# Kernel optimization log

Measured on AMD Instinct MI355X. Metric: run time of the kernel, lower is better.

## Reference

```python
import jax, jax.numpy as jnp
import numpy as np

D = 8        # q_ndim (= dof_ndim)
HID = 200    # hidden_size
N = 16384    # batch of states
EPS = 0.1    # qdot regularizer coefficient in L()


def _lagrangian(z, Ws, bs):
    # z: (2D,) = [q, qdot]; angular_dims=() so CosSin is an identity pass-through
    v = z[D:]
    h = z
    for W, b in zip(Ws[:-1], bs[:-1]):
        h = jax.nn.softplus(h @ W + b)   # FCsoftplus blocks
    L = (h @ Ws[-1] + bs[-1])[0]          # final Linear -> scalar (Reshape(-1))
    return L + EPS * jnp.dot(v, v)


def setup_inputs():
    key = jax.random.key(0)
    ks = jax.random.split(key, 5)
    z = jax.random.normal(ks[0], (N, 2 * D), dtype=jnp.float32)
    t = jnp.zeros((), dtype=jnp.float32)

    def lin(k, fi, fo, scale):
        return (jax.random.normal(k, (fi, fo), dtype=jnp.float32)
                * jnp.float32(scale / np.sqrt(fi)))

    W0 = lin(ks[1], 2 * D, HID, 1.0)
    W1 = lin(ks[2], HID, HID, 1.0)
    W2 = lin(ks[3], HID, HID, 1.0)
    W3 = lin(ks[4], HID, 1, 0.01)  # small head keeps mass matrix M well conditioned
    b0 = jnp.zeros((HID,), jnp.float32)  # zero_bias init per FCsoftplus/Linear
    b1 = jnp.zeros((HID,), jnp.float32)
    b2 = jnp.zeros((HID,), jnp.float32)
    b3 = jnp.zeros((1,), jnp.float32)
    return dict(t=t, z=z, W0=W0, b0=b0, W1=W1, b1=b1, W2=W2, b2=b2, W3=W3, b3=b3)


def reference(t, z, W0, b0, W1, b1, W2, b2, W3, b3):
    # Euler-Lagrange dynamics (LagrangianDynamics):
    #   M a = dL/dq - (d2L/dq dv) v,  M = d2L/dv2;  dz/dt = [v, a]
    Ws = (W0, W1, W2, W3)
    bs = (b0, b1, b2, b3)
    Lfn = lambda zz: _lagrangian(zz, Ws, bs)

    def dyn_single(zi):
        g = jax.grad(Lfn)(zi)              # (2D,)  = [dL/dq, dL/dv]
        H = jax.jacfwd(jax.grad(Lfn))(zi)  # (2D,2D) Hessian of L wrt z
        v = zi[D:]
        M = H[D:, D:]                      # d(dL/dv)/dv  -> mass matrix
        C = H[D:, :D]                      # d(dL/dv)/dq
        F = g[:D] - C @ v
        a = jnp.linalg.solve(M, F)
        return jnp.concatenate([v, a])     # (2D,)

    return jax.vmap(dyn_single)(z)         # (N, 2D)
```

## Files before the change

### kernel.cpp

```cpp
#include <hip/hip_runtime.h>
#include <math.h>

#define DD 8
#define ZD 16
#define HID 200
#define EPSL 0.1f
#define BS 16
#define NTHREADS 1024
#define NKC 7
#define NMT 13
#define XSTR 216
#define CSTR 212
#define HSTR 20
#define WSTR 208
#define NTAN 8
#define NT4 4

#define KSC 1024.0f
#define SSC 64.0f
#define INV_K (1.0f/1024.0f)
#define INV_KS (1.0f/65536.0f)

typedef _Float16 half8 __attribute__((ext_vector_type(8)));
typedef _Float16 half4v __attribute__((ext_vector_type(4)));
typedef _Float16 half2v __attribute__((ext_vector_type(2)));
typedef __fp16 fp16x2 __attribute__((ext_vector_type(2)));
typedef float float4v __attribute__((ext_vector_type(4)));

#define S4 (NKC*NMT*64*8)
#define OFF_W1T 0
#define OFF_W2T (S4)
#define OFF_W1  (2*S4)
#define OFF_W2  (3*S4)
#define OFF_W0T (4*S4)
#define OFF_W0  (4*S4 + NMT*64*8)
#define WS_HALFS (4*S4 + NMT*64*8 + NKC*64*8)

__global__ void prep(const float* __restrict__ W0, const float* __restrict__ W1,
                     const float* __restrict__ W2, _Float16* __restrict__ ws)
{
    int idx = blockIdx.x * 256 + threadIdx.x;
    if (idx >= WS_HALFS) return;
    float v = 0.f;
    if (idx < 4*S4) {
        int arr = idx / S4, e = idx % S4;
        int kc = e / (NMT*64*8); int r = e % (NMT*64*8);
        int mt = r / (64*8); r %= 64*8;
        int lane = r / 8, j = r % 8;
        int m = mt*16 + (lane & 15);
        int k = kc*32 + (lane >> 4)*8 + j;
        if (m < HID && k < HID) {
            if      (arr == 0) v = W1[k*HID + m];
            else if (arr == 1) v = W2[k*HID + m];
            else if (arr == 2) v = W1[m*HID + k];
            else               v = W2[m*HID + k];
        }
    } else if (idx < OFF_W0) {
        int e = idx - OFF_W0T;
        int mt = e / (64*8); int r = e % (64*8);
        int lane = r / 8, j = r % 8;
        int m = mt*16 + (lane & 15);
        int k = (lane >> 4)*8 + j;
        if (m < HID && k < ZD) v = W0[k*HID + m];
    } else {
        int e = idx - OFF_W0;
        int kc = e / (64*8); int r = e % (64*8);
        int lane = r / 8, j = r % 8;
        int m = (lane & 15);
        int k = kc*32 + (lane >> 4)*8 + j;
        if (k < HID) v = W0[m*HID + k];
    }
    ws[idx] = (_Float16)v;
}

__device__ __forceinline__ half4v pk4(float4v a) {
    half2v lo = __builtin_bit_cast(half2v, __builtin_amdgcn_cvt_pkrtz(a.x, a.y));
    half2v hi = __builtin_bit_cast(half2v, __builtin_amdgcn_cvt_pkrtz(a.z, a.w));
    return __builtin_shufflevector(lo, hi, 0, 1, 2, 3);
}
__device__ __forceinline__ void sig_sp(float x, float& sp, float& sg) {
    float e = __expf(-fabsf(x));
    float r = 1.0f / (1.0f + e);
    sg = (x >= 0.f) ? r : (1.0f - r);
    sp = fmaxf(x, 0.f) + __logf(1.f + e);
}

template<int NTILES>
__device__ __forceinline__ void run_mv(const half8* __restrict__ Asw,
                                       const _Float16* __restrict__ Xsrc,
                                       int mt0, int mtc, int lane,
                                       float4v acc[2][NTILES])
{
    const int lm = lane & 15, q = lane >> 4;
#pragma unroll
    for (int m = 0; m < 2; ++m)
#pragma unroll
        for (int n = 0; n < NTILES; ++n)
            acc[m][n] = (float4v){0.f, 0.f, 0.f, 0.f};
    for (int kc = 0; kc < NKC; ++kc) {
        half8 a[2];
#pragma unroll
        for (int m = 0; m < 2; ++m)
            if (m < mtc) a[m] = Asw[(kc*NMT + mt0 + m)*64 + lane];
        half8 x[NTILES];
#pragma unroll
        for (int n = 0; n < NTILES; ++n)
            x[n] = *(const half8*)(Xsrc + (n*16 + lm)*XSTR + kc*32 + q*8);
#pragma unroll
        for (int m = 0; m < 2; ++m)
            if (m < mtc)
#pragma unroll
                for (int n = 0; n < NTILES; ++n)
                    acc[m][n] = __builtin_amdgcn_mfma_f32_16x16x32_f16(a[m], x[n], acc[m][n], 0, 0, 0);
    }
}

__global__ void __launch_bounds__(NTHREADS, 4)
lnn_main(const float* __restrict__ z,
         const float* __restrict__ W0, const float* __restrict__ b0,
         const float* __restrict__ b1, const float* __restrict__ b2,
         const float* __restrict__ W3,
         const _Float16* __restrict__ ws,
         float* __restrict__ out)
{
    __shared__ alignas(16) _Float16 Xt[128*XSTR];
    __shared__ alignas(16) _Float16 Xb[128*XSTR];
    __shared__ alignas(16) _Float16 Cf[5][16*CSTR];
    __shared__ alignas(16) _Float16 Xz[16*40];
    __shared__ alignas(16) _Float16 bsh[4*WSTR];
    __shared__ alignas(16) _Float16 w0t[NTAN*WSTR];
    __shared__ alignas(16) float gsh[16*HSTR];
    __shared__ alignas(16) float Hr[128*HSTR];

    const int tid  = threadIdx.x;
    const int wave = tid >> 6;
    const int lane = tid & 63;
    const int lm   = lane & 15;
    const int q    = lane >> 4;
    const int s0   = blockIdx.x * BS;

    const int twm  = wave >> 1;
    const int twn  = wave & 1;
    const int mt0t = (twm < 5) ? twm*2 : (twm + 5);
    const int mtct = (twm < 5) ? 2 : 1;

    const half8* W1Tsw = (const half8*)(ws + OFF_W1T);
    const half8* W2Tsw = (const half8*)(ws + OFF_W2T);
    const half8* W1sw  = (const half8*)(ws + OFF_W1);
    const half8* W2sw  = (const half8*)(ws + OFF_W2);
    const half8* W0Tsw = (const half8*)(ws + OFF_W0T);
    const half8* W0sw  = (const half8*)(ws + OFF_W0);

    if (tid < 256) {
        int s = tid >> 4, k = tid & 15;
        Xz[s*40 + k]      = (_Float16)z[(s0 + s)*ZD + k];
        Xz[s*40 + 16 + k] = (_Float16)0.f;
    }
    for (int idx = tid; idx < 128*16; idx += NTHREADS) {
        int r = idx >> 4, c = 200 + (idx & 15);
        Xt[r*XSTR + c] = (_Float16)0.f;
        Xb[r*XSTR + c] = (_Float16)0.f;
    }
    for (int idx = tid; idx < 4*WSTR; idx += NTHREADS) {
        int l = idx / WSTR, u = idx % WSTR;
        float v = 0.f;
        if (u < HID) {
            if      (l == 0) v = b0[u];
            else if (l == 1) v = b1[u];
            else if (l == 2) v = b2[u];
            else             v = KSC * W3[u];
        }
        bsh[idx] = (_Float16)v;
    }
    for (int idx = tid; idx < NTAN*WSTR; idx += NTHREADS) {
        int t = idx / WSTR, u = idx % WSTR;
        w0t[idx] = (_Float16)((u < HID) ? SSC * W0[(DD + t)*HID + u] : 0.f);
    }
    __syncthreads();

    float4v acc1[2][1];
    const int ubf = wave*16 + q*4;

    if (wave < NMT) {
        acc1[0][0] = (float4v){0.f,0.f,0.f,0.f};
        half8 xz = *(const half8*)(Xz + lm*40 + q*8);
        half8 a = W0Tsw[wave*64 + lane];
        acc1[0][0] = __builtin_amdgcn_mfma_f32_16x16x32_f16(a, xz, acc1[0][0], 0, 0, 0);
        half4v bb = *(const half4v*)(&bsh[0*WSTR + ubf]);
        float h[4], p[4];
#pragma unroll
        for (int r = 0; r < 4; ++r) {
            float av = acc1[0][0][r] + (float)bb[r];
            sig_sp(av, h[r], p[r]);
        }
        *(half4v*)(&Xt[lm*XSTR + ubf])     = pk4((float4v){h[0],h[1],h[2],h[3]});
        *(half4v*)(&Cf[0][lm*CSTR + ubf])  = pk4((float4v){p[0],p[1],p[2],p[3]});
    }
    __syncthreads();

    if (wave < NMT) run_mv<1>(W1Tsw, Xt, wave, 1, lane, acc1);
    __syncthreads();
    if (wave < NMT) {
        half4v bb = *(const half4v*)(&bsh[1*WSTR + ubf]);
        float h[4], p[4];
#pragma unroll
        for (int r = 0; r < 4; ++r) {
            float av = acc1[0][0][r] + (float)bb[r];
            sig_sp(av, h[r], p[r]);
        }
        *(half4v*)(&Xt[lm*XSTR + ubf])    = pk4((float4v){h[0],h[1],h[2],h[3]});
        *(half4v*)(&Cf[1][lm*CSTR + ubf]) = pk4((float4v){p[0],p[1],p[2],p[3]});
    }
    __syncthreads();

    if (wave < NMT) run_mv<1>(W2Tsw, Xt, wave, 1, lane, acc1);
    __syncthreads();
    if (wave < NMT) {
        half4v bb = *(const half4v*)(&bsh[2*WSTR + ubf]);
        half4v w3 = *(const half4v*)(&bsh[3*WSTR + ubf]);
        float d2[4], c2[4];
#pragma unroll
        for (int r = 0; r < 4; ++r) {
            float av = acc1[0][0][r] + (float)bb[r];
            float e = __expf(-fabsf(av));
            float rr = 1.f / (1.f + e);
            float sg = (av >= 0.f) ? rr : (1.f - rr);
            float wk = (float)w3[r];
            d2[r] = wk * sg;
            c2[r] = wk * sg * (1.f - sg);
        }
        *(half4v*)(&Xt[lm*XSTR + ubf])    = pk4((float4v){d2[0],d2[1],d2[2],d2[3]});
        *(half4v*)(&Cf[2][lm*CSTR + ubf]) = pk4((float4v){c2[0],c2[1],c2[2],c2[3]});
    }
    __syncthreads();

    if (wave < NMT) run_mv<1>(W2sw, Xt, wave, 1, lane, acc1);
    __syncthreads();
    if (wave < NMT) {
        half4v p1 = *(const half4v*)(&Cf[1][lm*CSTR + ubf]);
        half4v u1 = pk4(acc1[0][0]);
        half4v one = {(_Float16)1.f,(_Float16)1.f,(_Float16)1.f,(_Float16)1.f};
        *(half4v*)(&Xt[lm*XSTR + ubf])    = u1 * p1;
        *(half4v*)(&Cf[3][lm*CSTR + ubf]) = u1 * (one - p1);
    }
    __syncthreads();

    if (wave < NMT) run_mv<1>(W1sw, Xt, wave, 1, lane, acc1);
    __syncthreads();
    if (wave < NMT) {
        half4v p0 = *(const half4v*)(&Cf[0][lm*CSTR + ubf]);
        half4v u0 = pk4(acc1[0][0]);
        half4v one = {(_Float16)1.f,(_Float16)1.f,(_Float16)1.f,(_Float16)1.f};
        half4v d0 = u0 * p0;
        *(half4v*)(&Xt[lm*XSTR + ubf])    = d0;
        *(half4v*)(&Cf[4][lm*CSTR + ubf]) = d0 * (one - p0);
    }
    __syncthreads();

    if (wave == 0) {
        float4v g = (float4v){0.f,0.f,0.f,0.f};
        for (int kc = 0; kc < NKC; ++kc) {
            half8 a = W0sw[kc*64 + lane];
            half8 x = *(const half8*)(Xt + lm*XSTR + kc*32 + q*8);
            g = __builtin_amdgcn_mfma_f32_16x16x32_f16(a, x, g, 0, 0, 0);
        }
        float4v gv; gv.x = g.x*INV_K; gv.y = g.y*INV_K; gv.z = g.z*INV_K; gv.w = g.w*INV_K;
        *(float4v*)(&gsh[lm*HSTR + q*4]) = gv;
    } else {
        for (int idx = tid - 64; idx < 128*50; idx += NTHREADS - 64) {
            int row = idx / 50, u = (idx % 50)*4;
            int s = row & 15, t = row >> 4;
            half4v p0 = *(const half4v*)(&Cf[0][s*CSTR + u]);
            half4v w0 = *(const half4v*)(&w0t[t*WSTR + u]);
            *(half4v*)(&Xb[row*XSTR + u]) = p0 * w0;
        }
    }
    __syncthreads();

    float4v acc4[2][NT4];

    run_mv<NT4>(W1Tsw, Xb + twn*64*XSTR, mt0t, mtct, lane, acc4);
    __syncthreads();
#pragma unroll
    for (int m = 0; m < 2; ++m)
        if (m < mtct) {
            const int ub = (mt0t + m)*16 + q*4;
            half4v p1 = *(const half4v*)(&Cf[1][lm*CSTR + ub]);
#pragma unroll
            for (int n = 0; n < NT4; ++n) {
                int row = (twn*NT4 + n)*16 + lm;
                *(half4v*)(&Xt[row*XSTR + ub]) = pk4(acc4[m][n]) * p1;
            }
        }
    __syncthreads();

    run_mv<NT4>(W2Tsw, Xt + twn*64*XSTR, mt0t, mtct, lane, acc4);
    __syncthreads();
#pragma unroll
    for (int m = 0; m < 2; ++m)
        if (m < mtct) {
            const int ub = (mt0t + m)*16 + q*4;
            half4v c2 = *(const half4v*)(&Cf[2][lm*CSTR + ub]);
#pragma unroll
            for (int n = 0; n < NT4; ++n) {
                int row = (twn*NT4 + n)*16 + lm;
                *(half4v*)(&Xb[row*XSTR + ub]) = pk4(acc4[m][n]) * c2;
            }
        }
    __syncthreads();

    run_mv<NT4>(W2sw, Xb + twn*64*XSTR, mt0t, mtct, lane, acc4);
    __syncthreads();
#pragma unroll
    for (int m = 0; m < 2; ++m)
        if (m < mtct) {
            const int ub = (mt0t + m)*16 + q*4;
            half4v p1 = *(const half4v*)(&Cf[1][lm*CSTR + ub]);
            half4v c3 = *(const half4v*)(&Cf[3][lm*CSTR + ub]);
#pragma unroll
            for (int n = 0; n < NT4; ++n) {
                int row = (twn*NT4 + n)*16 + lm;
                half4v th1 = *(const half4v*)(&Xt[row*XSTR + ub]);
                *(half4v*)(&Xb[row*XSTR + ub]) = pk4(acc4[m][n]) * p1 + c3 * th1;
            }
        }
    __syncthreads();

    run_mv<NT4>(W1sw, Xb + twn*64*XSTR, mt0t, mtct, lane, acc4);
    __syncthreads();
#pragma unroll
    for (int m = 0; m < 2; ++m)
        if (m < mtct) {
            const int ub = (mt0t + m)*16 + q*4;
            half4v p0 = *(const half4v*)(&Cf[0][lm*CSTR + ub]);
            half4v c4 = *(const half4v*)(&Cf[4][lm*CSTR + ub]);
#pragma unroll
            for (int n = 0; n < NT4; ++n) {
                int row = (twn*NT4 + n)*16 + lm;
                half4v w0 = *(const half4v*)(&w0t[(twn*NT4 + n)*WSTR + ub]);
                *(half4v*)(&Xt[row*XSTR + ub]) = pk4(acc4[m][n]) * p0 + c4 * w0;
            }
        }
    __syncthreads();

    if (wave < 8) {
        float4v hacc = (float4v){0.f,0.f,0.f,0.f};
        for (int kc = 0; kc < NKC; ++kc) {
            half8 a = W0sw[kc*64 + lane];
            half8 x = *(const half8*)(Xt + (wave*16 + lm)*XSTR + kc*32 + q*8);
            hacc = __builtin_amdgcn_mfma_f32_16x16x32_f16(a, x, hacc, 0, 0, 0);
        }
        int row = wave*16 + lm;
        float4v hv;
        hv.x = hacc.x*INV_KS; hv.y = hacc.y*INV_KS;
        hv.z = hacc.z*INV_KS; hv.w = hacc.w*INV_KS;
        *(float4v*)(&Hr[row*HSTR + q*4]) = hv;
    }
    __syncthreads();

    if (tid < BS) {
        const int s = tid;
        float M[DD][DD], F[DD], v[DD], a[DD];
#pragma unroll
        for (int c = 0; c < DD; ++c) v[c] = z[(s0 + s)*ZD + DD + c];
#pragma unroll
        for (int r = 0; r < DD; ++r) {
            float f = gsh[s*HSTR + r];
#pragma unroll
            for (int c = 0; c < DD; ++c) {
                M[r][c] = Hr[(r*16 + s)*HSTR + DD + c] + ((r == c) ? 2.f*EPSL : 0.f);
                f -= Hr[(r*16 + s)*HSTR + c] * v[c];
            }
            F[r] = f;
        }
#pragma unroll
        for (int col = 0; col < DD; ++col) {
            const float inv = 1.f / M[col][col];
#pragma unroll
            for (int r = col + 1; r < DD; ++r) {
                const float fac = M[r][col] * inv;
#pragma unroll
                for (int c = col + 1; c < DD; ++c) M[r][c] -= fac * M[col][c];
                F[r] -= fac * F[col];
            }
        }
#pragma unroll
        for (int r = DD - 1; r >= 0; --r) {
            float ssum = F[r];
#pragma unroll
            for (int c = r + 1; c < DD; ++c) ssum -= M[r][c] * a[c];
            a[r] = ssum / M[r][r];
        }
        float* op = out + (size_t)(s0 + s)*ZD;
#pragma unroll
        for (int c = 0; c < DD; ++c) { op[c] = v[c]; op[DD + c] = a[c]; }
    }
}

extern "C" void kernel_launch(void* const* d_in, const int* in_sizes, int n_in,
                              void* d_out, int out_size, void* d_ws, size_t ws_size,
                              hipStream_t stream)
{
    const float* z  = (const float*)d_in[1];
    const float* W0 = (const float*)d_in[2];
    const float* b0 = (const float*)d_in[3];
    const float* W1 = (const float*)d_in[4];
    const float* b1 = (const float*)d_in[5];
    const float* W2 = (const float*)d_in[6];
    const float* b2 = (const float*)d_in[7];
    const float* W3 = (const float*)d_in[8];
    float* out = (float*)d_out;
    _Float16* ws = (_Float16*)d_ws;

    const int n = in_sizes[1] / (2*DD);

    prep<<<dim3((WS_HALFS + 255)/256), dim3(256), 0, stream>>>(W0, W1, W2, ws);
    lnn_main<<<dim3(n / BS), dim3(NTHREADS), 0, stream>>>(
        z, W0, b0, b1, b2, W3, ws, out);
}
```

Baseline: 159.9 us.

## Software-pipeline weight and activation loads in MFMA matvec and drop redundant barriers

The MFMA matvec helper is fully unrolled and now prefetches weight fragments several K-chunks ahead and activation fragments one chunk ahead. It is specialised on the M-tile count through a template parameter, so the runtime tile checks disappear. The W0 gradient and Hessian loops preload all weight fragments up front. Three barriers that separated tangent matvecs from their epilogues are removed, because each epilogue writes a buffer no other wave is reading at that point. The extra live registers may cause spills or lower occupancy under the existing launch bounds.

```diff
diff --git a/kernel.cpp b/kernel.cpp
--- a/kernel.cpp
+++ b/kernel.cpp
@@ -24,7 +24,6 @@
 typedef _Float16 half8 __attribute__((ext_vector_type(8)));
 typedef _Float16 half4v __attribute__((ext_vector_type(4)));
 typedef _Float16 half2v __attribute__((ext_vector_type(2)));
-typedef __fp16 fp16x2 __attribute__((ext_vector_type(2)));
 typedef float float4v __attribute__((ext_vector_type(4)));
 
 #define S4 (NKC*NMT*64*8)
@@ -85,33 +84,62 @@
     sp = fmaxf(x, 0.f) + __logf(1.f + e);
 }
 
-template<int NTILES>
+template<int NTILES, int MTC>
 __device__ __forceinline__ void run_mv(const half8* __restrict__ Asw,
                                        const _Float16* __restrict__ Xsrc,
-                                       int mt0, int mtc, int lane,
+                                       int mt0, int lane,
                                        float4v acc[2][NTILES])
 {
     const int lm = lane & 15, q = lane >> 4;
-#pragma unroll
-    for (int m = 0; m < 2; ++m)
+    constexpr int PF = (NTILES > 1) ? 3 : NKC;
+#pragma unroll
+    for (int m = 0; m < MTC; ++m)
 #pragma unroll
         for (int n = 0; n < NTILES; ++n)
             acc[m][n] = (float4v){0.f, 0.f, 0.f, 0.f};
+
+    half8 a[MTC][PF];
+#pragma unroll
+    for (int p = 0; p < PF; ++p)
+#pragma unroll
+        for (int m = 0; m < MTC; ++m)
+            a[m][p] = Asw[(p*NMT + mt0 + m)*64 + lane];
+
+    half8 x[NTILES];
+#pragma unroll
+    for (int n = 0; n < NTILES; ++n)
+        x[n] = *(const half8*)(Xsrc + (n*16 + lm)*XSTR + q*8);
+
+#pragma unroll
     for (int kc = 0; kc < NKC; ++kc) {
-        half8 a[2];
-#pragma unroll
-        for (int m = 0; m < 2; ++m)
-            if (m < mtc) a[m] = Asw[(kc*NMT + mt0 + m)*64 + lane];
-        half8 x[NTILES];
-#pragma unroll
-        for (int n = 0; n < NTILES; ++n)
-            x[n] = *(const half8*)(Xsrc + (n*16 + lm)*XSTR + kc*32 + q*8);
-#pragma unroll
-        for (int m = 0; m < 2; ++m)
-            if (m < mtc)
-#pragma unroll
-                for (int n = 0; n < NTILES; ++n)
-                    acc[m][n] = __builtin_amdgcn_mfma_f32_16x16x32_f16(a[m], x[n], acc[m][n], 0, 0, 0);
+        half8 xn[NTILES];
+        if (kc + 1 < NKC)
+#pragma unroll
+            for (int n = 0; n < NTILES; ++n)
+                xn[n] = *(const half8*)(Xsrc + (n*16 + lm)*XSTR + (kc+1)*32 + q*8);
+        half8 an[MTC];
+        if (kc + PF < NKC)
+#pragma unroll
+            for (int m = 0; m < MTC; ++m)
+                an[m] = Asw[((kc+PF)*NMT + mt0 + m)*64 + lane];
+
+#pragma unroll
+        for (int m = 0; m < MTC; ++m)
+#pragma unroll
+            for (int n = 0; n < NTILES; ++n)
+                acc[m][n] = __builtin_amdgcn_mfma_f32_16x16x32_f16(a[m][0], x[n], acc[m][n], 0, 0, 0);
+
+        if (kc + 1 < NKC) {
+#pragma unroll
+            for (int m = 0; m < MTC; ++m)
+#pragma unroll
+                for (int p = 0; p + 1 < PF; ++p) a[m][p] = a[m][p+1];
+            if (kc + PF < NKC)
+#pragma unroll
+                for (int m = 0; m < MTC; ++m) a[m][PF-1] = an[m];
+#pragma unroll
+            for (int n = 0; n < NTILES; ++n) x[n] = xn[n];
+        }
     }
 }
 
@@ -161,6 +189,10 @@
         Xt[r*XSTR + c] = (_Float16)0.f;
         Xb[r*XSTR + c] = (_Float16)0.f;
     }
+    if (tid < 8) {
+        Xt[16*XSTR + tid] = (_Float16)0.f;
+        Xb[16*XSTR + tid] = (_Float16)0.f;
+    }
     for (int idx = tid; idx < 4*WSTR; idx += NTHREADS) {
         int l = idx / WSTR, u = idx % WSTR;
         float v = 0.f;
@@ -198,7 +230,7 @@
     }
     __syncthreads();
 
-    if (wave < NMT) run_mv<1>(W1Tsw, Xt, wave, 1, lane, acc1);
+    if (wave < NMT) run_mv<1,1>(W1Tsw, Xt, wave, lane, acc1);
     __syncthreads();
     if (wave < NMT) {
         half4v bb = *(const half4v*)(&bsh[1*WSTR + ubf]);
@@ -213,7 +245,7 @@
     }
     __syncthreads();
 
-    if (wave < NMT) run_mv<1>(W2Tsw, Xt, wave, 1, lane, acc1);
+    if (wave < NMT) run_mv<1,1>(W2Tsw, Xt, wave, lane, acc1);
     __syncthreads();
     if (wave < NMT) {
         half4v bb = *(const half4v*)(&bsh[2*WSTR + ubf]);
@@ -234,7 +266,7 @@
     }
     __syncthreads();
 
-    if (wave < NMT) run_mv<1>(W2sw, Xt, wave, 1, lane, acc1);
+    if (wave < NMT) run_mv<1,1>(W2sw, Xt, wave, lane, acc1);
     __syncthreads();
     if (wave < NMT) {
         half4v p1 = *(const half4v*)(&Cf[1][lm*CSTR + ubf]);
@@ -245,7 +277,7 @@
     }
     __syncthreads();
 
-    if (wave < NMT) run_mv<1>(W1sw, Xt, wave, 1, lane, acc1);
+    if (wave < NMT) run_mv<1,1>(W1sw, Xt, wave, lane, acc1);
     __syncthreads();
     if (wave < NMT) {
         half4v p0 = *(const half4v*)(&Cf[0][lm*CSTR + ubf]);
@@ -258,11 +290,14 @@
     __syncthreads();
 
     if (wave == 0) {
+        half8 aw[NKC];
+#pragma unroll
+        for (int kc = 0; kc < NKC; ++kc) aw[kc] = W0sw[kc*64 + lane];
         float4v g = (float4v){0.f,0.f,0.f,0.f};
+#pragma unroll
         for (int kc = 0; kc < NKC; ++kc) {
-            half8 a = W0sw[kc*64 + lane];
             half8 x = *(const half8*)(Xt + lm*XSTR + kc*32 + q*8);
-            g = __builtin_amdgcn_mfma_f32_16x16x32_f16(a, x, g, 0, 0, 0);
+            g = __builtin_amdgcn_mfma_f32_16x16x32_f16(aw[kc], x, g, 0, 0, 0);
         }
         float4v gv; gv.x = g.x*INV_K; gv.y = g.y*INV_K; gv.z = g.z*INV_K; gv.w = g.w*INV_K;
         *(float4v*)(&gsh[lm*HSTR + q*4]) = gv;
@@ -279,8 +314,8 @@
 
     float4v acc4[2][NT4];
 
-    run_mv<NT4>(W1Tsw, Xb + twn*64*XSTR, mt0t, mtct, lane, acc4);
-    __syncthreads();
+    if (mtct == 2) run_mv<NT4,2>(W1Tsw, Xb + twn*64*XSTR, mt0t, lane, acc4);
+    else           run_mv<NT4,1>(W1Tsw, Xb + twn*64*XSTR, mt0t, lane, acc4);
 #pragma unroll
     for (int m = 0; m < 2; ++m)
         if (m < mtct) {
@@ -294,8 +329,8 @@
         }
     __syncthreads();
 
-    run_mv<NT4>(W2Tsw, Xt + twn*64*XSTR, mt0t, mtct, lane, acc4);
-    __syncthreads();
+    if (mtct == 2) run_mv<NT4,2>(W2Tsw, Xt + twn*64*XSTR, mt0t, lane, acc4);
+    else           run_mv<NT4,1>(W2Tsw, Xt + twn*64*XSTR, mt0t, lane, acc4);
 #pragma unroll
     for (int m = 0; m < 2; ++m)
         if (m < mtct) {
@@ -309,7 +344,8 @@
         }
     __syncthreads();
 
-    run_mv<NT4>(W2sw, Xb + twn*64*XSTR, mt0t, mtct, lane, acc4);
+    if (mtct == 2) run_mv<NT4,2>(W2sw, Xb + twn*64*XSTR, mt0t, lane, acc4);
+    else           run_mv<NT4,1>(W2sw, Xb + twn*64*XSTR, mt0t, lane, acc4);
     __syncthreads();
 #pragma unroll
     for (int m = 0; m < 2; ++m)
@@ -326,8 +362,8 @@
         }
     __syncthreads();
 
-    run_mv<NT4>(W1sw, Xb + twn*64*XSTR, mt0t, mtct, lane, acc4);
-    __syncthreads();
+    if (mtct == 2) run_mv<NT4,2>(W1sw, Xb + twn*64*XSTR, mt0t, lane, acc4);
+    else           run_mv<NT4,1>(W1sw, Xb + twn*64*XSTR, mt0t, lane, acc4);
 #pragma unroll
     for (int m = 0; m < 2; ++m)
         if (m < mtct) {
@@ -344,11 +380,14 @@
     __syncthreads();
 
     if (wave < 8) {
+        half8 aw[NKC];
+#pragma unroll
+        for (int kc = 0; kc < NKC; ++kc) aw[kc] = W0sw[kc*64 + lane];
         float4v hacc = (float4v){0.f,0.f,0.f,0.f};
+#pragma unroll
         for (int kc = 0; kc < NKC; ++kc) {
-            half8 a = W0sw[kc*64 + lane];
             half8 x = *(const half8*)(Xt + (wave*16 + lm)*XSTR + kc*32 + q*8);
-            hacc = __builtin_amdgcn_mfma_f32_16x16x32_f16(a, x, hacc, 0, 0, 0);
+            hacc = __builtin_amdgcn_mfma_f32_16x16x32_f16(aw[kc], x, hacc, 0, 0, 0);
         }
         int row = wave*16 + lm;
         float4v hv;
```

Result: no change. 160.1 us (+0.1%).
